# Optimization experiments

Measured on AMD Instinct MI355X. Metric: run time of the kernel, lower is better.

The kernel has to match this reference:

```python
import jax, jax.numpy as jnp
import numpy as np

N = 50000       # nodes
E = 800000      # edges (before self-loops)
IN_DIM = 128
HID = 64
HEADS = 4
C = HID // HEADS  # 16 per-head channels
NEG_SLOPE = 0.2   # PyG GATConv default
BN_EPS = 1e-5


def setup_inputs() -> dict:
    key = jax.random.key(0)
    ks = jax.random.split(key, 16)
    inp = {
        "x": jax.random.normal(ks[0], (N, IN_DIM), jnp.float32),
        "edge_index": jax.random.randint(ks[1], (2, E), 0, N, dtype=jnp.int32),
    }
    def glorot(k, shape):
        fan = sum(shape)
        return jax.random.normal(k, shape, jnp.float32) * jnp.sqrt(2.0 / fan)
    # layer 0: in=IN_DIM, layer 1: in=HID
    inp["W0"] = glorot(ks[2], (IN_DIM, HEADS * C))
    inp["a_src0"] = glorot(ks[3], (HEADS, C))
    inp["a_dst0"] = glorot(ks[4], (HEADS, C))
    inp["b0"] = jnp.zeros((HEADS * C,), jnp.float32)
    inp["g0"] = jnp.ones((HID,), jnp.float32)
    inp["be0"] = jnp.zeros((HID,), jnp.float32)
    inp["W1"] = glorot(ks[5], (HID, HEADS * C))
    inp["a_src1"] = glorot(ks[6], (HEADS, C))
    inp["a_dst1"] = glorot(ks[7], (HEADS, C))
    inp["b1"] = jnp.zeros((HEADS * C,), jnp.float32)
    inp["g1"] = jnp.ones((HID,), jnp.float32)
    inp["be1"] = jnp.zeros((HID,), jnp.float32)
    return inp


def _segment_softmax(e, dst, n):
    # softmax over edges grouped by destination node, per head. e: [Et, H]
    m = jax.ops.segment_max(e, dst, num_segments=n)          # [N, H]
    ex = jnp.exp(e - m[dst])
    s = jax.ops.segment_sum(ex, dst, num_segments=n)         # [N, H]
    return ex / (s[dst] + 1e-16)


def _gat_conv(h, src, dst, W, a_s, a_d, b):
    n = h.shape[0]
    hp = (h @ W).reshape(n, HEADS, C)                        # [N, H, C]
    al_s = jnp.einsum('nhc,hc->nh', hp, a_s)                 # [N, H]
    al_d = jnp.einsum('nhc,hc->nh', hp, a_d)
    e = jax.nn.leaky_relu(al_s[src] + al_d[dst], NEG_SLOPE)  # [Et, H]
    alpha = _segment_softmax(e, dst, n)
    msg = hp[src] * alpha[:, :, None]                        # [Et, H, C]
    out = jax.ops.segment_sum(msg, dst, num_segments=n)      # [N, H, C]
    return out.reshape(n, HEADS * C) + b


def _batch_norm(h, g, b):
    mu = h.mean(axis=0)
    var = h.var(axis=0)
    return (h - mu) * jax.lax.rsqrt(var + BN_EPS) * g + b


def reference(x, edge_index, W0, a_src0, a_dst0, b0, g0, be0,
              W1, a_src1, a_dst1, b1, g1, be1):
    n = x.shape[0]
    loops = jnp.arange(n, dtype=edge_index.dtype)
    src = jnp.concatenate([edge_index[0], loops])  # PyG adds self-loops
    dst = jnp.concatenate([edge_index[1], loops])
    h = _gat_conv(x, src, dst, W0, a_src0, a_dst0, b0)
    h = _batch_norm(h, g0, be0)
    h = jax.nn.relu(h)  # dropout: identity (eval / deterministic)
    h = _gat_conv(h, src, dst, W1, a_src1, a_dst1, b1)
    h = _batch_norm(h, g1, be1)
    return h
```

## Files before the change

kernel.cpp:

```cpp
#include <hip/hip_runtime.h>
#include <hip/hip_fp16.h>

#define CAP 64

__device__ __forceinline__ float sel4(float4 v, int h) {
  return h == 0 ? v.x : h == 1 ? v.y : h == 2 ? v.z : v.w;
}

template<int K, bool APPLY_BN>
__global__ void __launch_bounds__(256, 4)
gemm_tiled(const float* __restrict__ X, const float* __restrict__ W,
           const float* __restrict__ a_s, const float* __restrict__ a_d,
           const float* __restrict__ bnsum, const float* __restrict__ bnsq,
           const float* __restrict__ g, const float* __restrict__ be,
           __half* __restrict__ hp, float* __restrict__ al_s,
           float* __restrict__ al_d, int n)
{
  __shared__ float Wl[(K / 4) * 64 * 4];
  __shared__ float Xt[64 * K];

  for (int gi = threadIdx.x; gi < (K / 4) * 64; gi += 256) {
    int k4 = gi >> 6, ln = gi & 63;
    float4 w;
    w.x = W[(k4 * 4 + 0) * 64 + ln];
    w.y = W[(k4 * 4 + 1) * 64 + ln];
    w.z = W[(k4 * 4 + 2) * 64 + ln];
    w.w = W[(k4 * 4 + 3) * 64 + ln];
    *(float4*)&Wl[gi * 4] = w;
  }

  int row0 = blockIdx.x * 64;
  int nrows = min(64, n - row0);
  float4 sc, sh;
  if (APPLY_BN) {
    int cg = (threadIdx.x & 15) * 4;
    float inv_n = 1.f / (float)n;
#pragma unroll
    for (int q = 0; q < 4; ++q) {
      float mu  = bnsum[cg + q] * inv_n;
      float var = bnsq[cg + q] * inv_n - mu * mu;
      float s   = g[cg + q] * rsqrtf(var + 1e-5f);
      ((float*)&sc)[q] = s;
      ((float*)&sh)[q] = be[cg + q] - mu * s;
    }
  }
  const float4* src = (const float4*)(X + (size_t)row0 * K);
  int nf4 = nrows * (K / 4);
  for (int i = threadIdx.x; i < nf4; i += 256) {
    float4 v = src[i];
    if (APPLY_BN) {
      v.x = fmaxf(v.x * sc.x + sh.x, 0.f);
      v.y = fmaxf(v.y * sc.y + sh.y, 0.f);
      v.z = fmaxf(v.z * sc.z + sh.z, 0.f);
      v.w = fmaxf(v.w * sc.w + sh.w, 0.f);
    }
    *(float4*)&Xt[i * 4] = v;
  }
  __syncthreads();

  int lane = threadIdx.x & 63;
  int wid  = threadIdx.x >> 6;
  int rbase = wid * 16;
  float acc[16];
#pragma unroll
  for (int r = 0; r < 16; ++r) acc[r] = 0.f;

  for (int k4 = 0; k4 < K / 4; ++k4) {
    float4 wv = *(const float4*)&Wl[(k4 * 64 + lane) * 4];
#pragma unroll
    for (int r = 0; r < 16; ++r) {
      float4 xv = *(const float4*)&Xt[(rbase + r) * K + k4 * 4];
      acc[r] += xv.x * wv.x + xv.y * wv.y + xv.z * wv.z + xv.w * wv.w;
    }
  }

  float as_l = a_s[lane], ad_l = a_d[lane];
  int h = lane >> 4, c = lane & 15;
#pragma unroll
  for (int r = 0; r < 16; ++r) {
    int lr = rbase + r;
    if (lr >= nrows) break;
    int row = row0 + lr;
    float a = acc[r];
    hp[(size_t)row * 64 + lane] = __float2half(a);
    float vs = a * as_l;
    float vd = a * ad_l;
#pragma unroll
    for (int off = 8; off >= 1; off >>= 1) {
      vs += __shfl_xor(vs, off, 64);
      vd += __shfl_xor(vd, off, 64);
    }
    if (c == 0) { al_s[row * 4 + h] = vs; al_d[row * 4 + h] = vd; }
  }
}

__global__ void hist_k(const int* __restrict__ ei, int E, int N, int* __restrict__ count)
{
  int e = blockIdx.x * 256 + threadIdx.x;
  int Et = E + N;
  if (e >= Et) return;
  int d = (e < E) ? ei[E + e] : (e - E);
  atomicAdd(&count[d], 1);
}

__global__ void scan_block_k(const int* __restrict__ count, int* __restrict__ row_ptr,
                             int* __restrict__ partial, int* __restrict__ done_ctr,
                             int nb, int n)
{
  __shared__ int woff[16];
  __shared__ int is_last;
  int tid = threadIdx.x;
  int i = blockIdx.x * 1024 + tid;
  int v = (i < n) ? count[i] : 0;
  int lane = tid & 63, wid = tid >> 6;
  int incl = v;
#pragma unroll
  for (int off = 1; off < 64; off <<= 1) {
    int t = __shfl_up(incl, off, 64);
    if (lane >= off) incl += t;
  }
  if (lane == 63) woff[wid] = incl;
  __syncthreads();
  if (tid < 16) {
    int wv = woff[tid];
    int winc = wv;
#pragma unroll
    for (int off = 1; off < 16; off <<= 1) {
      int t = __shfl_up(winc, off, 64);
      if (tid >= off) winc += t;
    }
    woff[tid] = winc - wv;
    if (tid == 15) partial[blockIdx.x] = winc;
  }
  __syncthreads();
  if (i < n) row_ptr[i] = woff[wid] + incl - v;

  __threadfence();
  if (tid == 0) is_last = (atomicAdd(done_ctr, 1) == nb - 1) ? 1 : 0;
  __syncthreads();
  if (is_last && tid < 64) {
    int pv = (tid < nb) ? partial[tid] : 0;
    int pincl = pv;
#pragma unroll
    for (int off = 1; off < 64; off <<= 1) {
      int t = __shfl_up(pincl, off, 64);
      if (tid >= off) pincl += t;
    }
    if (tid < nb) partial[tid] = pincl - pv;
    if (tid == 63) row_ptr[n] = pincl;
    __threadfence();
  }
}

__global__ void scan_add_k(int* __restrict__ row_ptr, int* __restrict__ cursor,
                           const int* __restrict__ partial, int n)
{
  int i = blockIdx.x * 1024 + threadIdx.x;
  if (i < n) {
    int r = row_ptr[i] + partial[blockIdx.x];
    row_ptr[i] = r;
    cursor[i] = r;
  }
}

__global__ void scatter_k(const int* __restrict__ ei, int E, int N,
                          int* __restrict__ cursor, int* __restrict__ col_src)
{
  int e = blockIdx.x * 256 + threadIdx.x;
  int Et = E + N;
  if (e >= Et) return;
  int s, d;
  if (e < E) { s = ei[e]; d = ei[E + e]; } else { s = d = e - E; }
  int pos = atomicAdd(&cursor[d], 1);
  col_src[pos] = s;
}

__global__ void __launch_bounds__(256)
node_agg(const int* __restrict__ row_ptr, const int* __restrict__ col_src,
         const float* __restrict__ al_s, const float* __restrict__ al_d,
         const __half* __restrict__ hp, const float* __restrict__ bias,
         float* __restrict__ hpre, float* __restrict__ bnsum, float* __restrict__ bnsq,
         int n)
{
  __shared__ int   sh_s[4][CAP];
  __shared__ float sh_w[4][CAP * 4];
  __shared__ float sh_o[4][64];
  __shared__ float shs[64], shq[64];

  int lane = threadIdx.x & 63;
  int wid  = threadIdx.x >> 6;
  int c    = lane & 31;
  int e2   = lane >> 5;
  int h4   = c >> 3;
  float b  = bias[lane];
  float lsum = 0.f, lsq = 0.f;
  int nwaves = gridDim.x * 4;

  for (int d = blockIdx.x * 4 + wid; d < n; d += nwaves) {
    int beg = row_ptr[d], end = row_ptr[d + 1];
    int deg = end - beg;
    float4 ald4 = *(const float4*)(al_d + (size_t)d * 4);
    float p0 = 0.f, p1 = 0.f, p2 = 0.f, p3 = 0.f;
    float acc0 = 0.f, acc1 = 0.f;
    float outv;

    if (deg <= CAP) {
      int degR = (deg + 1) & ~1;
      if (lane < deg) {
        int s = __builtin_nontemporal_load(&col_src[beg + lane]);
        float4 a = *(const float4*)(al_s + (size_t)s * 4);
        float ex = a.x + ald4.x; ex = ex >= 0.f ? ex : 0.2f * ex;
        float ey = a.y + ald4.y; ey = ey >= 0.f ? ey : 0.2f * ey;
        float ez = a.z + ald4.z; ez = ez >= 0.f ? ez : 0.2f * ez;
        float ew = a.w + ald4.w; ew = ew >= 0.f ? ew : 0.2f * ew;
        ex = __expf(ex); ey = __expf(ey); ez = __expf(ez); ew = __expf(ew);
        sh_s[wid][lane] = s;
        *(float4*)&sh_w[wid][lane * 4] = make_float4(ex, ey, ez, ew);
        p0 = ex; p1 = ey; p2 = ez; p3 = ew;
      } else if (lane < degR) {
        sh_s[wid][lane] = 0;
        *(float4*)&sh_w[wid][lane * 4] = make_float4(0.f, 0.f, 0.f, 0.f);
      }
      __builtin_amdgcn_wave_barrier();

      int j = 0;
      for (; j + 16 <= degR; j += 16) {
#pragma unroll
        for (int k = 0; k < 8; ++k) {
          int e = j + k * 2 + e2;
          int s = sh_s[wid][e];
          float wh = sh_w[wid][e * 4 + h4];
          unsigned raw = *(const unsigned*)(hp + (size_t)s * 64 + c * 2);
          float2 f = __half22float2(*(const __half2*)&raw);
          acc0 += wh * f.x;
          acc1 += wh * f.y;
        }
      }
      for (; j < degR; j += 2) {
        int e = j + e2;
        int s = sh_s[wid][e];
        float wh = sh_w[wid][e * 4 + h4];
        unsigned raw = *(const unsigned*)(hp + (size_t)s * 64 + c * 2);
        float2 f = __half22float2(*(const __half2*)&raw);
        acc0 += wh * f.x;
        acc1 += wh * f.y;
      }
      acc0 += __shfl_xor(acc0, 32, 64);
      acc1 += __shfl_xor(acc1, 32, 64);

#pragma unroll
      for (int off = 32; off >= 1; off >>= 1) {
        p0 += __shfl_xor(p0, off, 64);
        p1 += __shfl_xor(p1, off, 64);
        p2 += __shfl_xor(p2, off, 64);
        p3 += __shfl_xor(p3, off, 64);
      }

      if (lane < 32) *(float2*)&sh_o[wid][c * 2] = make_float2(acc0, acc1);
      __builtin_amdgcn_wave_barrier();
      float den = (lane < 16) ? p0 : (lane < 32) ? p1 : (lane < 48) ? p2 : p3;
      outv = sh_o[wid][lane] / (den + 1e-16f) + b;
    } else {
      for (int j = beg; j < end; ++j) {
        int s = col_src[j];
        float4 a = *(const float4*)(al_s + (size_t)s * 4);
        float ex = a.x + ald4.x; ex = ex >= 0.f ? ex : 0.2f * ex;
        float ey = a.y + ald4.y; ey = ey >= 0.f ? ey : 0.2f * ey;
        float ez = a.z + ald4.z; ez = ez >= 0.f ? ez : 0.2f * ez;
        float ew = a.w + ald4.w; ew = ew >= 0.f ? ew : 0.2f * ew;
        ex = __expf(ex); ey = __expf(ey); ez = __expf(ez); ew = __expf(ew);
        p0 += ex; p1 += ey; p2 += ez; p3 += ew;
        float wh = sel4(make_float4(ex, ey, ez, ew), h4);
        unsigned raw = *(const unsigned*)(hp + (size_t)s * 64 + c * 2);
        float2 f = __half22float2(*(const __half2*)&raw);
        acc0 += wh * f.x;
        acc1 += wh * f.y;
      }
      acc0 += __shfl_xor(acc0, 32, 64);
      acc1 += __shfl_xor(acc1, 32, 64);
      if (lane < 32) *(float2*)&sh_o[wid][c * 2] = make_float2(acc0, acc1);
      __builtin_amdgcn_wave_barrier();
      float den = (lane < 16) ? p0 : (lane < 32) ? p1 : (lane < 48) ? p2 : p3;
      outv = sh_o[wid][lane] / (den + 1e-16f) + b;
    }

    __builtin_nontemporal_store(outv, &hpre[(size_t)d * 64 + lane]);
    lsum += outv; lsq += outv * outv;
  }

  if (threadIdx.x < 64) { shs[threadIdx.x] = 0.f; shq[threadIdx.x] = 0.f; }
  __syncthreads();
  atomicAdd(&shs[lane], lsum);
  atomicAdd(&shq[lane], lsq);
  __syncthreads();
  if (threadIdx.x < 64) {
    atomicAdd(&bnsum[threadIdx.x], shs[threadIdx.x]);
    atomicAdd(&bnsq[threadIdx.x],  shq[threadIdx.x]);
  }
}

__global__ void bn_apply(float* __restrict__ buf, const float* __restrict__ bnsum,
                         const float* __restrict__ bnsq, const float* __restrict__ g,
                         const float* __restrict__ be, int n)
{
  size_t i = (size_t)blockIdx.x * 256 + threadIdx.x;
  size_t total = (size_t)n * 64;
  if (i >= total) return;
  int c = (int)(i & 63);
  float inv_n = 1.f / (float)n;
  float mu  = bnsum[c] * inv_n;
  float var = bnsq[c] * inv_n - mu * mu;
  buf[i] = (buf[i] - mu) * rsqrtf(var + 1e-5f) * g[c] + be[c];
}

extern "C" void kernel_launch(void* const* d_in, const int* in_sizes, int n_in,
                              void* d_out, int out_size, void* d_ws, size_t ws_size,
                              hipStream_t stream) {
  const float* x   = (const float*)d_in[0];
  const int*   ei  = (const int*)d_in[1];
  const float* W0  = (const float*)d_in[2];
  const float* as0 = (const float*)d_in[3];
  const float* ad0 = (const float*)d_in[4];
  const float* b0  = (const float*)d_in[5];
  const float* g0  = (const float*)d_in[6];
  const float* be0 = (const float*)d_in[7];
  const float* W1  = (const float*)d_in[8];
  const float* as1 = (const float*)d_in[9];
  const float* ad1 = (const float*)d_in[10];
  const float* b1  = (const float*)d_in[11];
  const float* g1  = (const float*)d_in[12];
  const float* be1 = (const float*)d_in[13];
  float* out = (float*)d_out;

  int N = in_sizes[0] / 128;
  int E = in_sizes[1] / 2;
  int Et = E + N;

  char* w = (char*)d_ws;
  auto alloc = [&](size_t bytes) {
    char* p = w; w += (bytes + 255) & ~255ull; return p;
  };
  int*    count = (int*)alloc((size_t)N * 4 + 4 * 64 * 4 + 4);
  float*  bnsum0 = (float*)(count + N);
  float*  bnsq0  = bnsum0 + 64;
  float*  bnsum1 = bnsq0 + 64;
  float*  bnsq1  = bnsum1 + 64;
  int*    done_ctr = (int*)(bnsq1 + 64);
  __half* hp    = (__half*)alloc((size_t)N * 64 * 2);
  float*  hpre0 = (float*)alloc((size_t)N * 64 * 4);
  float*  als   = (float*)alloc((size_t)N * 4 * 4);
  float*  ald   = (float*)alloc((size_t)N * 4 * 4);
  int*    rowp  = (int*)alloc((size_t)(N + 1) * 4);
  int*    cursor= (int*)alloc((size_t)N * 4);
  int*    parts = (int*)alloc(64 * 4);
  int*    csrc  = (int*)alloc((size_t)Et * 4);

  dim3 blk(256);
  int gEt   = (Et + 255) / 256;
  int gN64  = (N * 64 + 255) / 256;
  int nb    = (N + 1023) / 1024;
  int gTile = (N + 63) / 64;

  hipMemsetAsync(count, 0, (size_t)N * 4 + 4 * 64 * 4 + 4, stream);

  hist_k<<<gEt, blk, 0, stream>>>(ei, E, N, count);
  scan_block_k<<<nb, 1024, 0, stream>>>(count, rowp, parts, done_ctr, nb, N);
  scan_add_k<<<nb, 1024, 0, stream>>>(rowp, cursor, parts, N);
  scatter_k<<<gEt, blk, 0, stream>>>(ei, E, N, cursor, csrc);

  gemm_tiled<128, false><<<gTile, blk, 0, stream>>>(x, W0, as0, ad0,
                                                    nullptr, nullptr, nullptr, nullptr,
                                                    hp, als, ald, N);
  node_agg<<<2048, blk, 0, stream>>>(rowp, csrc, als, ald, hp, b0,
                                     hpre0, bnsum0, bnsq0, N);

  gemm_tiled<64, true><<<gTile, blk, 0, stream>>>(hpre0, W1, as1, ad1,
                                                  bnsum0, bnsq0, g0, be0,
                                                  hp, als, ald, N);
  node_agg<<<2048, blk, 0, stream>>>(rowp, csrc, als, ald, hp, b1,
                                     out, bnsum1, bnsq1, N);
  bn_apply<<<gN64, blk, 0, stream>>>(out, bnsum1, bnsq1, g1, be1, N);
}
```

Before: 359.9 us.

## Prefetch first 32 neighbor features into registers before softmax weight computation

For low-degree nodes, the aggregation kernel now issues the gathers of half-precision neighbor features for the first 32 edges into registers before it computes the attention logits and exponentials. The aim is to overlap gather latency with the al_s loads and exp math instead of running them one after the other. Padding moves to multiples of 16, and the fast-path degree cap rises from 64 to 128 by looping the weight computation over 64-lane chunks. In exchange it uses about 32 extra registers per lane, which may lower occupancy, and it adds more masked loads and zero-padding writes for small degrees.

```diff
diff --git a/kernel.cpp b/kernel.cpp
--- a/kernel.cpp
+++ b/kernel.cpp
@@ -1,7 +1,7 @@
 #include <hip/hip_runtime.h>
 #include <hip/hip_fp16.h>
 
-#define CAP 64
+#define CAP 128
 
 __device__ __forceinline__ float sel4(float4 v, int h) {
   return h == 0 ? v.x : h == 1 ? v.y : h == 2 ? v.z : v.w;
@@ -205,45 +205,63 @@
     float outv;
 
     if (deg <= CAP) {
-      int degR = (deg + 1) & ~1;
-      if (lane < deg) {
-        int s = __builtin_nontemporal_load(&col_src[beg + lane]);
-        float4 a = *(const float4*)(al_s + (size_t)s * 4);
-        float ex = a.x + ald4.x; ex = ex >= 0.f ? ex : 0.2f * ex;
-        float ey = a.y + ald4.y; ey = ey >= 0.f ? ey : 0.2f * ey;
-        float ez = a.z + ald4.z; ez = ez >= 0.f ? ez : 0.2f * ez;
-        float ew = a.w + ald4.w; ew = ew >= 0.f ? ew : 0.2f * ew;
-        ex = __expf(ex); ey = __expf(ey); ez = __expf(ez); ew = __expf(ew);
-        sh_s[wid][lane] = s;
-        *(float4*)&sh_w[wid][lane * 4] = make_float4(ex, ey, ez, ew);
-        p0 = ex; p1 = ey; p2 = ez; p3 = ew;
-      } else if (lane < degR) {
-        sh_s[wid][lane] = 0;
-        *(float4*)&sh_w[wid][lane * 4] = make_float4(0.f, 0.f, 0.f, 0.f);
+      int degR = (deg + 15) & ~15;
+      int R = min(degR, 32);
+
+      int sreg[16];
+#pragma unroll
+      for (int t = 0; t < 16; ++t) {
+        int e = t * 2 + e2;
+        sreg[t] = (e < deg) ? col_src[beg + e] : 0;
+      }
+      unsigned raw[16];
+#pragma unroll
+      for (int t = 0; t < 16; ++t) {
+        int e = t * 2 + e2;
+        raw[t] = (e < R) ? *(const unsigned*)(hp + (size_t)sreg[t] * 64 + c * 2) : 0u;
+      }
+
+      for (int jb = 0; jb < degR; jb += 64) {
+        int jj = jb + lane;
+        if (jj < deg) {
+          int s = col_src[beg + jj];
+          float4 a = *(const float4*)(al_s + (size_t)s * 4);
+          float ex = a.x + ald4.x; ex = ex >= 0.f ? ex : 0.2f * ex;
+          float ey = a.y + ald4.y; ey = ey >= 0.f ? ey : 0.2f * ey;
+          float ez = a.z + ald4.z; ez = ez >= 0.f ? ez : 0.2f * ez;
+          float ew = a.w + ald4.w; ew = ew >= 0.f ? ew : 0.2f * ew;
+          ex = __expf(ex); ey = __expf(ey); ez = __expf(ez); ew = __expf(ew);
+          sh_s[wid][jj] = s;
+          *(float4*)&sh_w[wid][jj * 4] = make_float4(ex, ey, ez, ew);
+          p0 += ex; p1 += ey; p2 += ez; p3 += ew;
+        } else if (jj < degR) {
+          sh_s[wid][jj] = 0;
+          *(float4*)&sh_w[wid][jj * 4] = make_float4(0.f, 0.f, 0.f, 0.f);
+        }
       }
       __builtin_amdgcn_wave_barrier();
 
-      int j = 0;
-      for (; j + 16 <= degR; j += 16) {
+#pragma unroll
+      for (int t = 0; t < 16; ++t) {
+        int e = t * 2 + e2;
+        if (e < R) {
+          float wh = sh_w[wid][e * 4 + h4];
+          float2 f = __half22float2(*(const __half2*)&raw[t]);
+          acc0 += wh * f.x;
+          acc1 += wh * f.y;
+        }
+      }
+      for (int j = 32; j < degR; j += 16) {
 #pragma unroll
         for (int k = 0; k < 8; ++k) {
           int e = j + k * 2 + e2;
           int s = sh_s[wid][e];
           float wh = sh_w[wid][e * 4 + h4];
-          unsigned raw = *(const unsigned*)(hp + (size_t)s * 64 + c * 2);
-          float2 f = __half22float2(*(const __half2*)&raw);
+          unsigned rr = *(const unsigned*)(hp + (size_t)s * 64 + c * 2);
+          float2 f = __half22float2(*(const __half2*)&rr);
           acc0 += wh * f.x;
           acc1 += wh * f.y;
         }
-      }
-      for (; j < degR; j += 2) {
-        int e = j + e2;
-        int s = sh_s[wid][e];
-        float wh = sh_w[wid][e * 4 + h4];
-        unsigned raw = *(const unsigned*)(hp + (size_t)s * 64 + c * 2);
-        float2 f = __half22float2(*(const __half2*)&raw);
-        acc0 += wh * f.x;
-        acc1 += wh * f.y;
       }
       acc0 += __shfl_xor(acc0, 32, 64);
       acc1 += __shfl_xor(acc1, 32, 64);
@@ -271,8 +289,8 @@
         ex = __expf(ex); ey = __expf(ey); ez = __expf(ez); ew = __expf(ew);
         p0 += ex; p1 += ey; p2 += ez; p3 += ew;
         float wh = sel4(make_float4(ex, ey, ez, ew), h4);
-        unsigned raw = *(const unsigned*)(hp + (size_t)s * 64 + c * 2);
-        float2 f = __half22float2(*(const __half2*)&raw);
+        unsigned rr = *(const unsigned*)(hp + (size_t)s * 64 + c * 2);
+        float2 f = __half22float2(*(const __half2*)&rr);
         acc0 += wh * f.x;
         acc1 += wh * f.y;
       }
```

Result: slower. 376.2 us (+4.5%).
